# Performance work log

Hardware: AMD Instinct MI355X
Metric: run time of the kernel (lower is better)

The kernel has to match this reference:

```python
import jax, jax.numpy as jnp
import numpy as np

DIM = 192; HEADS = 6
RES = (8, 96, 180)      # (Pl, Lat, Lon), all divisible by window -> pad/crop are no-ops
WIN = (2, 6, 12)        # (win_pl, win_lat, win_lon)
SHIFT = (1, 3, 6)
MLP_RATIO = 4


def earth_position_index(win):
    wpl, wlat, wlon = win
    zi = np.arange(wpl); zj = -np.arange(wpl) * wpl
    hi = np.arange(wlat); hj = -np.arange(wlat) * wlat
    w = np.arange(wlon)
    c1 = np.stack(np.meshgrid(zi, hi, w, indexing='ij')).reshape(3, -1)
    c2 = np.stack(np.meshgrid(zj, hj, w, indexing='ij')).reshape(3, -1)
    coords = (c1[:, :, None] - c2[:, None, :]).transpose(1, 2, 0).copy()  # (N, N, 3)
    coords[:, :, 2] += wlon - 1
    coords[:, :, 1] *= 2 * wlon - 1
    coords[:, :, 0] *= (2 * wlon - 1) * wlat * wlat
    return coords.sum(-1)  # (N, N) int index into bias table


def shift_window_mask(res, win, shift):
    Pl, Lat, Lon = res; wpl, wlat, wlon = win; spl, slat, slon = shift
    m = np.zeros((Pl, Lat, Lon + slon))
    cnt = 0
    pls = (slice(0, -wpl), slice(-wpl, -spl), slice(-spl, None))
    las = (slice(0, -wlat), slice(-wlat, -slat), slice(-slat, None))
    los = (slice(0, -wlon), slice(-wlon, -slon), slice(-slon, None))
    for p in pls:
        for l in las:
            for o in los:
                m[p, l, o] = cnt; cnt += 1
    m = m[:, :, :Lon]
    npl, nlat, nlon = Pl // wpl, Lat // wlat, Lon // wlon
    mw = m.reshape(npl, wpl, nlat, wlat, nlon, wlon).transpose(4, 0, 2, 1, 3, 5)
    mw = mw.reshape(nlon, npl * nlat, wpl * wlat * wlon)
    am = mw[:, :, None, :] - mw[:, :, :, None]
    return np.where(am != 0, -100.0, 0.0).astype(np.float32)  # (nlon, nW, N, N)


EPI = earth_position_index(WIN)                       # static int index
ATTN_MASK = shift_window_mask(RES, WIN, SHIFT)        # static float mask


def setup_inputs() -> dict:
    key = jax.random.key(0)
    ks = jax.random.split(key, 16)
    Pl, Lat, Lon = RES; wpl, wlat, wlon = WIN
    L = Pl * Lat * Lon
    nW = (Pl // wpl) * (Lat // wlat)  # type_of_windows
    tbl = wpl ** 2 * wlat ** 2 * (2 * wlon - 1)
    C = DIM; H = MLP_RATIO * DIM
    n = lambda k, s, std=0.02: (jax.random.normal(k, s, dtype=jnp.float32) * std)
    return {
        'x': jax.random.normal(ks[0], (1, L, C), dtype=jnp.float32),
        'norm1_g': jnp.ones((C,), jnp.float32), 'norm1_b': jnp.zeros((C,), jnp.float32),
        'qkv_w': n(ks[1], (C, 3 * C)), 'qkv_b': jnp.zeros((3 * C,), jnp.float32),
        'bias_table': n(ks[2], (tbl, nW, HEADS)),
        'proj_w': n(ks[3], (C, C)), 'proj_b': jnp.zeros((C,), jnp.float32),
        'norm2_g': jnp.ones((C,), jnp.float32), 'norm2_b': jnp.zeros((C,), jnp.float32),
        'fc1_w': n(ks[4], (C, H)), 'fc1_b': jnp.zeros((H,), jnp.float32),
        'fc2_w': n(ks[5], (H, C)), 'fc2_b': jnp.zeros((C,), jnp.float32),
    }


def _layernorm(y, g, b, eps=1e-5):
    mu = y.mean(-1, keepdims=True)
    var = y.var(-1, keepdims=True)
    return (y - mu) / jnp.sqrt(var + eps) * g + b


def reference(x, norm1_g, norm1_b, qkv_w, qkv_b, bias_table, proj_w, proj_b,
              norm2_g, norm2_b, fc1_w, fc1_b, fc2_w, fc2_b):
    B, L, C = x.shape
    Pl, Lat, Lon = RES; wpl, wlat, wlon = WIN; spl, slat, slon = SHIFT
    npl, nlat, nlon = Pl // wpl, Lat // wlat, Lon // wlon
    N = wpl * wlat * wlon; nW = npl * nlat
    h = HEADS; d = C // h
    scale = d ** -0.5

    shortcut = x
    y = _layernorm(x, norm1_g, norm1_b).reshape(B, Pl, Lat, Lon, C)
    y = jnp.roll(y, shift=(-spl, -slat, -slon), axis=(1, 2, 3))
    # window partition: b (npl wpl)(nlat wlat)(nlon wlon) c -> (b nlon)(npl nlat)(wpl wlat wlon) c
    yw = y.reshape(B, npl, wpl, nlat, wlat, nlon, wlon, C)
    yw = yw.transpose(0, 5, 1, 3, 2, 4, 6, 7).reshape(B * nlon, nW, N, C)

    qkv = (yw @ qkv_w + qkv_b).reshape(B * nlon, nW, N, 3, h, d)
    qkv = qkv.transpose(3, 0, 4, 1, 2, 5)  # (3, B_, h, nW, N, d)
    q, k, v = qkv[0] * scale, qkv[1], qkv[2]
    attn = jnp.einsum('bhwnd,bhwmd->bhwnm', q, k)  # (B_, h, nW, N, N)

    bias = bias_table[EPI.reshape(-1)].reshape(N, N, nW, h).transpose(3, 2, 0, 1)  # (h, nW, N, N)
    attn = attn + bias[None]
    mask = jnp.asarray(ATTN_MASK)  # (nlon, nW, N, N)
    attn = attn.reshape(B, nlon, h, nW, N, N) + mask[None, :, None]
    attn = jax.nn.softmax(attn.reshape(B * nlon, h, nW, N, N), axis=-1)

    out = jnp.einsum('bhwnm,bhwmd->bhwnd', attn, v)
    out = out.transpose(0, 2, 3, 1, 4).reshape(B * nlon, nW, N, C)
    out = out @ proj_w + proj_b
    # window reverse + un-shift
    out = out.reshape(B, nlon, npl, nlat, wpl, wlat, wlon, C)
    out = out.transpose(0, 2, 4, 3, 5, 1, 6, 7).reshape(B, Pl, Lat, Lon, C)
    out = jnp.roll(out, shift=(spl, slat, slon), axis=(1, 2, 3)).reshape(B, L, C)

    x = shortcut + out
    y = _layernorm(x, norm2_g, norm2_b)
    y = jax.nn.gelu(y @ fc1_w + fc1_b, approximate=False) @ fc2_w + fc2_b
    return x + y
```

## Files before the change

### kernel.cpp

```cpp
#include <hip/hip_runtime.h>


typedef __attribute__((ext_vector_type(8))) short short8;
typedef __attribute__((ext_vector_type(4))) short short4v;
typedef __attribute__((ext_vector_type(4))) float floatx4;
typedef unsigned short bfu;

#define GLOAD_LDS16(g, l)                                            \
  __builtin_amdgcn_global_load_lds(                                  \
      (const __attribute__((address_space(1))) unsigned int*)(g),    \
      (__attribute__((address_space(3))) unsigned int*)(l), 16, 0, 0)

__device__ __forceinline__ bfu f2bf(float f) {
  unsigned int u = __builtin_bit_cast(unsigned int, f);
  u += 0x7fffu + ((u >> 16) & 1u);
  return (bfu)(u >> 16);
}
__device__ __forceinline__ float bf2f(bfu s) {
  return __builtin_bit_cast(float, (unsigned int)s << 16);
}

__global__ void wt_kernel(const float* __restrict__ src, bfu* __restrict__ dst,
                          int K, int N) {
  int idx = blockIdx.x * 256 + threadIdx.x;
  if (idx >= K * N) return;
  int k = idx / N, n = idx % N;
  dst[(size_t)n * K + k] = f2bf(src[idx]);
}

__global__ void bias2_kernel(const float* __restrict__ table,
                             bfu* __restrict__ out) {
  int idx = blockIdx.x * 256 + threadIdx.x;
  if (idx >= 1271808) return;
  int h = idx / 211968;
  int r = idx % 211968;
  int w = r / 3312, ep = r % 3312;
  out[idx] = f2bf(table[(size_t)ep * 384 + w * 6 + h]);
}

__global__ void vpad_kernel(unsigned int* __restrict__ vbw) {
  int tid = threadIdx.x;
  int dd = tid >> 3, c = tid & 7;
  vbw[(size_t)blockIdx.x * 2560 + dd * 80 + 72 + c] = 0;
}

__global__ __launch_bounds__(256) void ln1_kernel(
    const float* __restrict__ x, const float* __restrict__ g,
    const float* __restrict__ be, bfu* __restrict__ A1) {
  int wv = threadIdx.x >> 6, lane = threadIdx.x & 63;
  int r = blockIdx.x * 4 + wv;
  int n = r % 144, w = (r / 144) & 63, bb = r / 9216;
  int ip = w >> 4, il = w & 15;
  int p1 = n / 72, rem = n % 72, l1 = rem / 12, o1 = rem % 12;
  int pl = ip * 2 + p1 + 1;   if (pl >= 8) pl -= 8;
  int lat = il * 6 + l1 + 3;  if (lat >= 96) lat -= 96;
  int lon = bb * 12 + o1 + 6; if (lon >= 180) lon -= 180;
  size_t t = (size_t)(pl * 96 + lat) * 180 + lon;
  const float* xr = x + t * 192;
  float v0 = xr[lane], v1 = xr[lane + 64], v2 = xr[lane + 128];
  float s = v0 + v1 + v2;
  #pragma unroll
  for (int o = 32; o; o >>= 1) s += __shfl_xor(s, o);
  float mu = s * (1.0f / 192.0f);
  float d0 = v0 - mu, d1 = v1 - mu, d2 = v2 - mu;
  float q2 = d0 * d0 + d1 * d1 + d2 * d2;
  #pragma unroll
  for (int o = 32; o; o >>= 1) q2 += __shfl_xor(q2, o);
  float rstd = rsqrtf(q2 * (1.0f / 192.0f) + 1e-5f);
  bfu* orow = A1 + (size_t)r * 192;
  orow[lane]       = f2bf(d0 * rstd * g[lane]       + be[lane]);
  orow[lane + 64]  = f2bf(d1 * rstd * g[lane + 64]  + be[lane + 64]);
  orow[lane + 128] = f2bf(d2 * rstd * g[lane + 128] + be[lane + 128]);
}

__global__ __launch_bounds__(256) void ln2_kernel(
    const float* __restrict__ xin, const float* __restrict__ g,
    const float* __restrict__ be, bfu* __restrict__ yout) {
  int wv = threadIdx.x >> 6, lane = threadIdx.x & 63;
  size_t r = (size_t)blockIdx.x * 4 + wv;
  const float* xr = xin + r * 192;
  float v0 = xr[lane], v1 = xr[lane + 64], v2 = xr[lane + 128];
  float s = v0 + v1 + v2;
  #pragma unroll
  for (int o = 32; o; o >>= 1) s += __shfl_xor(s, o);
  float mu = s * (1.0f / 192.0f);
  float d0 = v0 - mu, d1 = v1 - mu, d2 = v2 - mu;
  float q2 = d0 * d0 + d1 * d1 + d2 * d2;
  #pragma unroll
  for (int o = 32; o; o >>= 1) q2 += __shfl_xor(q2, o);
  float rstd = rsqrtf(q2 * (1.0f / 192.0f) + 1e-5f);
  bfu* orow = yout + r * 192;
  orow[lane]       = f2bf(d0 * rstd * g[lane]       + be[lane]);
  orow[lane + 64]  = f2bf(d1 * rstd * g[lane + 64]  + be[lane + 64]);
  orow[lane + 128] = f2bf(d2 * rstd * g[lane + 128] + be[lane + 128]);
}

__global__ __launch_bounds__(256, 4) void gemm_kernel(
    const bfu* __restrict__ A, const bfu* __restrict__ BT,
    const float* __restrict__ bias, int K, int NT, int mode,
    const float* aux, void* out0, void* out1, void* out2) {
  __shared__ __align__(16) short LB[14336];
  short* As = LB;
  short* Bs = LB + 8192;
  bfu* E = (bfu*)LB;
  const int tid = threadIdx.x;
  const int wv = tid >> 6, lane = tid & 63;
  const int r16 = lane & 15, quad = lane >> 4;
  const int sw = r16 & 7;

  const int W = gridDim.x;
  const int work = (blockIdx.x & 7) * (W >> 3) + (blockIdx.x >> 3);
  const int m0 = (work / NT) * 128;
  const int n0 = (work % NT) * 96;
  const bfu* Bsrc = BT + (size_t)n0 * K;

  floatx4 acc[2][6];
  #pragma unroll
  for (int s = 0; s < 2; ++s)
    #pragma unroll
    for (int j = 0; j < 6; ++j) acc[s][j] = (floatx4){0.f, 0.f, 0.f, 0.f};

  for (int kc = 0; kc < K; kc += 64) {
    __syncthreads();
    #pragma unroll
    for (int j = 0; j < 4; ++j) {
      int c = j * 256 + tid;
      int row = c >> 3, l = (c & 7) ^ (row & 7);
      GLOAD_LDS16(A + (size_t)(m0 + row) * K + kc + l * 8, As + c * 8);
    }
    #pragma unroll
    for (int j = 0; j < 3; ++j) {
      int c = j * 256 + tid;
      int row = c >> 3, l = (c & 7) ^ (row & 7);
      GLOAD_LDS16(Bsrc + (size_t)row * K + kc + l * 8, Bs + c * 8);
    }
    __syncthreads();
    #pragma unroll
    for (int ks = 0; ks < 2; ++ks) {
      const int p8 = ((ks * 4 + quad) ^ sw) * 8;
      short8 a[2], b[6];
      #pragma unroll
      for (int s = 0; s < 2; ++s)
        a[s] = *(const short8*)(As + (wv * 32 + s * 16 + r16) * 64 + p8);
      #pragma unroll
      for (int j = 0; j < 6; ++j)
        b[j] = *(const short8*)(Bs + (j * 16 + r16) * 64 + p8);
      #pragma unroll
      for (int s = 0; s < 2; ++s)
        #pragma unroll
        for (int j = 0; j < 6; ++j)
          acc[s][j] =
              __builtin_amdgcn_mfma_f32_16x16x32_bf16(a[s], b[j], acc[s][j], 0, 0, 0);
    }
  }

  if (mode == 0 || mode == 2) {
    __syncthreads();
    #pragma unroll
    for (int s = 0; s < 2; ++s) {
      int er = wv * 32 + s * 16 + quad * 4;
      #pragma unroll
      for (int j = 0; j < 6; ++j) {
        int c = j * 16 + r16;
        float bia = bias[n0 + c];
        #pragma unroll
        for (int i = 0; i < 4; ++i) {
          float val = acc[s][j][i] + bia;
          if (mode == 0) {
            if (n0 < 192) val *= 0.17677669529663687f;
            E[(er + i) * 104 + c] = f2bf(val);
          } else {
            float ge = 0.5f * val * (1.0f + erff(val * 0.70710678118654752f));
            E[(er + i) * 104 + c] = f2bf(ge);
          }
        }
      }
    }
    __syncthreads();
    if (mode == 2) {
      #pragma unroll
      for (int u = 0; u < 6; ++u) {
        int id = u * 256 + tid;
        int r = id / 12, c8 = (id % 12) * 8;
        *(short8*)((bfu*)out0 + (size_t)(m0 + r) * 768 + n0 + c8) =
            *(const short8*)(E + r * 104 + c8);
      }
    } else if (n0 < 384) {
      bfu* dst = (bfu*)(n0 < 192 ? out0 : out1);
      #pragma unroll
      for (int u = 0; u < 6; ++u) {
        int id = u * 256 + tid;
        int r = id / 12, c8 = (id % 12) * 8;
        int row = m0 + r;
        int n = row % 144, w = (row / 144) & 63, bb = row / 9216;
        int head = ((n0 + c8) % 192) >> 5, dd = c8 & 31;
        size_t win = (size_t)(bb * 6 + head) * 64 + w;
        *(short8*)(dst + win * 4608 + n * 32 + dd) =
            *(const short8*)(E + r * 104 + c8);
      }
    } else {
      #pragma unroll
      for (int u = 0; u < 6; ++u) {
        int id = u * 256 + tid;
        int c = id % 96, k8 = id / 96;
        int r0 = k8 * 8;
        int row0 = m0 + r0;
        int n = row0 % 144, w = (row0 / 144) & 63, bb = row0 / 9216;
        int head = ((n0 + c) % 192) >> 5, dd = c & 31;
        size_t win = (size_t)(bb * 6 + head) * 64 + w;
        short8 t8;
        #pragma unroll
        for (int i = 0; i < 8; ++i) t8[i] = (short)E[(r0 + i) * 104 + c];
        *(short8*)((bfu*)out2 + win * 5120 + dd * 160 + n) = t8;
      }
    }
  } else {
    #pragma unroll
    for (int s = 0; s < 2; ++s) {
      const int row0 = m0 + wv * 32 + s * 16 + quad * 4;
      #pragma unroll
      for (int j = 0; j < 6; ++j) {
        int col = n0 + j * 16 + r16;
        float bia = bias[col];
        #pragma unroll
        for (int i = 0; i < 4; ++i) {
          int row = row0 + i;
          float val = acc[s][j][i] + bia;
          if (mode == 1) {
            int n = row % 144, w = (row / 144) & 63, bb = row / 9216;
            int ip = w >> 4, il = w & 15;
            int p1 = n / 72, rem = n % 72, l1 = rem / 12, o1 = rem % 12;
            int pl = ip * 2 + p1 + 1;   if (pl >= 8) pl -= 8;
            int lat = il * 6 + l1 + 3;  if (lat >= 96) lat -= 96;
            int lon = bb * 12 + o1 + 6; if (lon >= 180) lon -= 180;
            size_t t = (size_t)(pl * 96 + lat) * 180 + lon;
            ((float*)out0)[t * 192 + col] = aux[t * 192 + col] + val;
          } else {
            size_t idx = (size_t)row * 192 + col;
            ((float*)out0)[idx] = aux[idx] + val;
          }
        }
      }
    }
  }
}

__global__ __launch_bounds__(256) void attn_kernel(
    const bfu* __restrict__ qg_, const bfu* __restrict__ kg_,
    const bfu* __restrict__ vg_, const bfu* __restrict__ tblT,
    bfu* __restrict__ aout) {
  __shared__ __align__(16) bfu Ss[144 * 148];
  __shared__ __align__(16) bfu bias_l[3312];
  __shared__ unsigned short rn[144];
  __shared__ short cm[144];
  __shared__ unsigned char regs[144];

  const int w = blockIdx.x, h0 = blockIdx.y * 2, b = blockIdx.z;
  const int tid = threadIdx.x;
  const int wv = tid >> 6, lane = tid & 63, r16 = lane & 15, quad = lane >> 4;

  if (tid < 144) {
    int n = tid;
    int p1 = n / 72, rem = n % 72, l1 = rem / 12, o1 = rem % 12;
    rn[n] = (unsigned short)(828 * p1 + 23 * l1 + o1 + 11);
    cm[n] = (short)(1656 * p1 + 138 * l1 - o1);
    int ip = w >> 4, il = w & 15;
    int pl = ip * 2 + p1, lat = il * 6 + l1, lon = b * 12 + o1;
    int rp = pl < 6 ? 0 : (pl < 7 ? 1 : 2);
    int rl = lat < 90 ? 0 : (lat < 93 ? 1 : 2);
    int ro = lon < 174 ? 0 : 1;
    regs[n] = (unsigned char)(rp * 9 + rl * 3 + ro);
  }

  {
    const bfu* bsrc = tblT + (size_t)(h0 * 64 + w) * 3312;
    GLOAD_LDS16(bsrc + tid * 8, bias_l + tid * 8);
    if (tid < 158) GLOAD_LDS16(bsrc + (256 + tid) * 8, bias_l + (256 + tid) * 8);
  }

  short4v ov[2][5];
  #pragma unroll
  for (int hh = 0; hh < 2; ++hh) {
    const int h = h0 + hh;
    const size_t win = (size_t)((b * 6 + h) * 64 + w);
    const bfu* qg = qg_ + win * 4608;
    const bfu* kg = kg_ + win * 4608;
    const bfu* vt = vg_ + win * 5120;

    #pragma unroll 3
    for (int u = 0; u < 21; ++u) {
      int t = wv * 21 + u;
      if (t < 81) {
        int tn = t / 9, tm = t % 9;
        short8 a  = *(const short8*)(qg + (tn * 16 + r16) * 32 + quad * 8);
        short8 bo = *(const short8*)(kg + (tm * 16 + r16) * 32 + quad * 8);
        floatx4 z = (floatx4){0.f, 0.f, 0.f, 0.f};
        floatx4 d = __builtin_amdgcn_mfma_f32_16x16x32_bf16(a, bo, z, 0, 0, 0);
        int m = tm * 16 + r16;
        #pragma unroll
        for (int i = 0; i < 4; ++i)
          Ss[(tn * 16 + quad * 4 + i) * 148 + m] = f2bf(d[i]);
      }
    }
    __syncthreads();

    for (int rb = 0; rb < 9; ++rb) {
      int rr = rb * 16 + wv * 4 + quad;
      unsigned char rgn = regs[rr];
      int rnv = rn[rr];
      const bfu* srow = Ss + rr * 148;
      float v[9];
      float mx = -1e30f;
      #pragma unroll
      for (int j = 0; j < 9; ++j) {
        int c = r16 + 16 * j;
        float s = bf2f(srow[c]) + bf2f(bias_l[rnv + cm[c]]);
        if (regs[c] != rgn) s -= 100.0f;
        v[j] = s;
        mx = fmaxf(mx, s);
      }
      #pragma unroll
      for (int o = 8; o; o >>= 1) mx = fmaxf(mx, __shfl_xor(mx, o));
      float sum = 0.f;
      #pragma unroll
      for (int j = 0; j < 9; ++j) { v[j] = __expf(v[j] - mx); sum += v[j]; }
      #pragma unroll
      for (int o = 8; o; o >>= 1) sum += __shfl_xor(sum, o);
      float inv = 1.0f / sum;
      bfu* wrow = Ss + rr * 148;
      #pragma unroll
      for (int j = 0; j < 9; ++j) wrow[r16 + 16 * j] = f2bf(v[j] * inv);
    }
    __syncthreads();

    if (hh == 0) {
      const bfu* bsrc = tblT + (size_t)((h0 + 1) * 64 + w) * 3312;
      GLOAD_LDS16(bsrc + tid * 8, bias_l + tid * 8);
      if (tid < 158) GLOAD_LDS16(bsrc + (256 + tid) * 8, bias_l + (256 + tid) * 8);
    }

    short8 bfr[2][5];
    #pragma unroll
    for (int td = 0; td < 2; ++td)
      #pragma unroll
      for (int km = 0; km < 5; ++km)
        bfr[td][km] =
            *(const short8*)(vt + (td * 16 + r16) * 160 + km * 32 + quad * 8);

    #pragma unroll
    for (int u = 0; u < 5; ++u) {
      int t = wv * 5 + u;
      if (t < 18) {
        int tn = t >> 1, td = t & 1;
        floatx4 acc = (floatx4){0.f, 0.f, 0.f, 0.f};
        #pragma unroll
        for (int km = 0; km < 5; ++km) {
          short8 a;
          if (km == 4 && quad >= 2) {
            a = (short8)(short)0;
          } else {
            const bfu* ap = Ss + (tn * 16 + r16) * 148 + km * 32 + quad * 8;
            *(short4v*)&a       = *(const short4v*)ap;
            *((short4v*)&a + 1) = *(const short4v*)(ap + 4);
          }
          acc = __builtin_amdgcn_mfma_f32_16x16x32_bf16(bfr[td][km], a, acc, 0, 0, 0);
        }
        short4v o;
        #pragma unroll
        for (int i = 0; i < 4; ++i) o[i] = (short)f2bf(acc[i]);
        ov[hh][u] = o;
      }
    }
    if (hh == 0) __syncthreads();
  }

  __syncthreads();
  bfu* Os = Ss;
  #pragma unroll
  for (int u = 0; u < 5; ++u) {
    int t = wv * 5 + u;
    if (t < 18) {
      int tn = t >> 1, td = t & 1;
      int ro = tn * 16 + r16;
      *(short4v*)(Os + ro * 80 + td * 16 + quad * 4)      = ov[0][u];
      *(short4v*)(Os + ro * 80 + 32 + td * 16 + quad * 4) = ov[1][u];
    }
  }
  __syncthreads();
  const size_t obase = (size_t)((b * 64 + w) * 144) * 192 + h0 * 32;
  #pragma unroll
  for (int u = 0; u < 5; ++u) {
    int c = u * 256 + tid;
    if (c < 1152) {
      int r = c >> 3, k = c & 7;
      *(short8*)(aout + obase + (size_t)r * 192 + k * 8) =
          *(const short8*)(Os + r * 80 + k * 8);
    }
  }
}

extern "C" void kernel_launch(void* const* d_in, const int* in_sizes, int n_in,
                              void* d_out, int out_size, void* d_ws, size_t ws_size,
                              hipStream_t stream) {
  (void)in_sizes; (void)n_in; (void)out_size; (void)ws_size;
  const float* x     = (const float*)d_in[0];
  const float* n1g   = (const float*)d_in[1];
  const float* n1b   = (const float*)d_in[2];
  const float* qkvw  = (const float*)d_in[3];
  const float* qkvb  = (const float*)d_in[4];
  const float* tbl   = (const float*)d_in[5];
  const float* projw = (const float*)d_in[6];
  const float* projb = (const float*)d_in[7];
  const float* n2g   = (const float*)d_in[8];
  const float* n2b   = (const float*)d_in[9];
  const float* fc1w  = (const float*)d_in[10];
  const float* fc1b  = (const float*)d_in[11];
  const float* fc2w  = (const float*)d_in[12];
  const float* fc2b  = (const float*)d_in[13];

  char* ws = (char*)d_ws;
  bfu* wt_qkv   = (bfu*)(ws + 0);
  bfu* wt_proj  = (bfu*)(ws + 221184);
  bfu* wt_fc1   = (bfu*)(ws + 294912);
  bfu* wt_fc2   = (bfu*)(ws + 589824);
  bfu* tblT     = (bfu*)(ws + 884736);
  bfu* A1       = (bfu*)(ws + 16809984);
  bfu* qb       = (bfu*)(ws + 69894144);
  bfu* kb       = (bfu*)(ws + 122978304);
  bfu* vb       = (bfu*)(ws + 176062464);
  bfu* hb       = qb;
  float* out    = (float*)d_out;

  wt_kernel<<<432, 256, 0, stream>>>(qkvw, wt_qkv, 192, 576);
  wt_kernel<<<144, 256, 0, stream>>>(projw, wt_proj, 192, 192);
  wt_kernel<<<576, 256, 0, stream>>>(fc1w, wt_fc1, 192, 768);
  wt_kernel<<<576, 256, 0, stream>>>(fc2w, wt_fc2, 768, 192);
  bias2_kernel<<<4968, 256, 0, stream>>>(tbl, tblT);
  vpad_kernel<<<5760, 256, 0, stream>>>((unsigned int*)vb);
  ln1_kernel<<<34560, 256, 0, stream>>>(x, n1g, n1b, A1);
  gemm_kernel<<<6480, 256, 0, stream>>>(A1, wt_qkv, qkvb, 192, 6, 0,
                                        nullptr, qb, kb, vb);
  attn_kernel<<<dim3(64, 3, 15), 256, 0, stream>>>(qb, kb, vb, tblT, A1);
  gemm_kernel<<<2160, 256, 0, stream>>>(A1, wt_proj, projb, 192, 2, 1,
                                        x, out, nullptr, nullptr);
  ln2_kernel<<<34560, 256, 0, stream>>>(out, n2g, n2b, A1);
  gemm_kernel<<<8640, 256, 0, stream>>>(A1, wt_fc1, fc1b, 192, 8, 2,
                                        nullptr, hb, nullptr, nullptr);
  gemm_kernel<<<2160, 256, 0, stream>>>(hb, wt_fc2, fc2b, 768, 2, 3,
                                        out, out, nullptr, nullptr);
}
```

Before: 967.7 us.

## Fold log2e into scores, drop softmax max pass, restructure GEMM and QK tiling

Premultiplies the q scale and the bias table by log2(e) so softmax uses exp2 directly, and removes the max-subtraction pass, assuming scores stay in a safe range. The GEMM now loads A straight into registers from global memory and stages only B in LDS with a K-chunk of 192, with occupancy lowered to 3. The QK^T stage keeps q fragments in registers and gives each wave fixed key tiles. Column mask and bias offsets are hoisted into registers. Dropping the max subtraction risks overflow for larger logits, and the bigger register footprint reduces occupancy.

Result: slower. 987.9 us (+2.1%).

```diff
diff --git a/kernel.cpp b/kernel.cpp
--- a/kernel.cpp
+++ b/kernel.cpp
@@ -35,7 +35,7 @@
   int h = idx / 211968;
   int r = idx % 211968;
   int w = r / 3312, ep = r % 3312;
-  out[idx] = f2bf(table[(size_t)ep * 384 + w * 6 + h]);
+  out[idx] = f2bf(table[(size_t)ep * 384 + w * 6 + h] * 1.4426950408889634f);
 }
 
 __global__ void vpad_kernel(unsigned int* __restrict__ vbw) {
@@ -95,14 +95,12 @@
   orow[lane + 128] = f2bf(d2 * rstd * g[lane + 128] + be[lane + 128]);
 }
 
-__global__ __launch_bounds__(256, 4) void gemm_kernel(
+__global__ __launch_bounds__(256, 3) void gemm_kernel(
     const bfu* __restrict__ A, const bfu* __restrict__ BT,
     const float* __restrict__ bias, int K, int NT, int mode,
     const float* aux, void* out0, void* out1, void* out2) {
-  __shared__ __align__(16) short LB[14336];
-  short* As = LB;
-  short* Bs = LB + 8192;
-  bfu* E = (bfu*)LB;
+  __shared__ __align__(16) short Bs[18432];
+  bfu* E = (bfu*)Bs;
   const int tid = threadIdx.x;
   const int wv = tid >> 6, lane = tid & 63;
   const int r16 = lane & 15, quad = lane >> 4;
@@ -114,43 +112,46 @@
   const int n0 = (work % NT) * 96;
   const bfu* Bsrc = BT + (size_t)n0 * K;
 
+  const short* Arow[2];
+  #pragma unroll
+  for (int s = 0; s < 2; ++s)
+    Arow[s] = (const short*)A + (size_t)(m0 + wv * 32 + s * 16 + r16) * K + quad * 8;
+
   floatx4 acc[2][6];
   #pragma unroll
   for (int s = 0; s < 2; ++s)
     #pragma unroll
     for (int j = 0; j < 6; ++j) acc[s][j] = (floatx4){0.f, 0.f, 0.f, 0.f};
 
-  for (int kc = 0; kc < K; kc += 64) {
-    __syncthreads();
-    #pragma unroll
-    for (int j = 0; j < 4; ++j) {
+  for (int kc = 0; kc < K; kc += 192) {
+    __syncthreads();
+    #pragma unroll
+    for (int j = 0; j < 9; ++j) {
       int c = j * 256 + tid;
-      int row = c >> 3, l = (c & 7) ^ (row & 7);
-      GLOAD_LDS16(A + (size_t)(m0 + row) * K + kc + l * 8, As + c * 8);
-    }
-    #pragma unroll
-    for (int j = 0; j < 3; ++j) {
-      int c = j * 256 + tid;
-      int row = c >> 3, l = (c & 7) ^ (row & 7);
+      int row = c / 24, sl = c % 24;
+      int l = (sl & ~7) | ((sl ^ row) & 7);
       GLOAD_LDS16(Bsrc + (size_t)row * K + kc + l * 8, Bs + c * 8);
     }
-    __syncthreads();
-    #pragma unroll
-    for (int ks = 0; ks < 2; ++ks) {
-      const int p8 = ((ks * 4 + quad) ^ sw) * 8;
-      short8 a[2], b[6];
-      #pragma unroll
-      for (int s = 0; s < 2; ++s)
-        a[s] = *(const short8*)(As + (wv * 32 + s * 16 + r16) * 64 + p8);
+    short8 ar[2][6];
+    #pragma unroll
+    for (int s = 0; s < 2; ++s)
+      #pragma unroll
+      for (int ks = 0; ks < 6; ++ks)
+        ar[s][ks] = *(const short8*)(Arow[s] + kc + ks * 32);
+    __syncthreads();
+    #pragma unroll
+    for (int ks = 0; ks < 6; ++ks) {
+      const int s_log = ks * 4 + quad;
+      const int p8 = ((s_log & ~7) | ((s_log ^ sw) & 7)) * 8;
+      short8 b[6];
       #pragma unroll
       for (int j = 0; j < 6; ++j)
-        b[j] = *(const short8*)(Bs + (j * 16 + r16) * 64 + p8);
-      #pragma unroll
-      for (int s = 0; s < 2; ++s)
-        #pragma unroll
-        for (int j = 0; j < 6; ++j)
-          acc[s][j] =
-              __builtin_amdgcn_mfma_f32_16x16x32_bf16(a[s], b[j], acc[s][j], 0, 0, 0);
+        b[j] = *(const short8*)(Bs + (j * 16 + r16) * 192 + p8);
+      #pragma unroll
+      for (int j = 0; j < 6; ++j) {
+        acc[0][j] = __builtin_amdgcn_mfma_f32_16x16x32_bf16(ar[0][ks], b[j], acc[0][j], 0, 0, 0);
+        acc[1][j] = __builtin_amdgcn_mfma_f32_16x16x32_bf16(ar[1][ks], b[j], acc[1][j], 0, 0, 0);
+      }
     }
   }
 
@@ -167,7 +168,7 @@
         for (int i = 0; i < 4; ++i) {
           float val = acc[s][j][i] + bia;
           if (mode == 0) {
-            if (n0 < 192) val *= 0.17677669529663687f;
+            if (n0 < 192) val *= 0.25503633958871686f;
             E[(er + i) * 104 + c] = f2bf(val);
           } else {
             float ge = 0.5f * val * (1.0f + erff(val * 0.70710678118654752f));
@@ -277,6 +278,16 @@
     GLOAD_LDS16(bsrc + tid * 8, bias_l + tid * 8);
     if (tid < 158) GLOAD_LDS16(bsrc + (256 + tid) * 8, bias_l + (256 + tid) * 8);
   }
+  __syncthreads();
+
+  short cmv[9];
+  unsigned char creg[9];
+  #pragma unroll
+  for (int j = 0; j < 9; ++j) {
+    int c = r16 + 16 * j;
+    cmv[j] = cm[c];
+    creg[j] = regs[c];
+  }
 
   short4v ov[2][5];
   #pragma unroll
@@ -287,19 +298,28 @@
     const bfu* kg = kg_ + win * 4608;
     const bfu* vt = vg_ + win * 5120;
 
-    #pragma unroll 3
-    for (int u = 0; u < 21; ++u) {
-      int t = wv * 21 + u;
-      if (t < 81) {
-        int tn = t / 9, tm = t % 9;
-        short8 a  = *(const short8*)(qg + (tn * 16 + r16) * 32 + quad * 8);
-        short8 bo = *(const short8*)(kg + (tm * 16 + r16) * 32 + quad * 8);
-        floatx4 z = (floatx4){0.f, 0.f, 0.f, 0.f};
-        floatx4 d = __builtin_amdgcn_mfma_f32_16x16x32_bf16(a, bo, z, 0, 0, 0);
-        int m = tm * 16 + r16;
-        #pragma unroll
-        for (int i = 0; i < 4; ++i)
-          Ss[(tn * 16 + quad * 4 + i) * 148 + m] = f2bf(d[i]);
+    short8 qf[9];
+    #pragma unroll
+    for (int t9 = 0; t9 < 9; ++t9)
+      qf[t9] = *(const short8*)(qg + (t9 * 16 + r16) * 32 + quad * 8);
+    const int tma = wv * 2, tmb = wv * 2 + 1;
+    short8 kfa = *(const short8*)(kg + (tma * 16 + r16) * 32 + quad * 8);
+    short8 kfb = *(const short8*)(kg + (tmb * 16 + r16) * 32 + quad * 8);
+    short8 kfc = *(const short8*)(kg + (128 + r16) * 32 + quad * 8);
+    const floatx4 z = (floatx4){0.f, 0.f, 0.f, 0.f};
+    #pragma unroll
+    for (int tn = 0; tn < 9; ++tn) {
+      bfu* srow = Ss + (tn * 16 + quad * 4) * 148;
+      floatx4 d = __builtin_amdgcn_mfma_f32_16x16x32_bf16(qf[tn], kfa, z, 0, 0, 0);
+      #pragma unroll
+      for (int i = 0; i < 4; ++i) srow[i * 148 + tma * 16 + r16] = f2bf(d[i]);
+      d = __builtin_amdgcn_mfma_f32_16x16x32_bf16(qf[tn], kfb, z, 0, 0, 0);
+      #pragma unroll
+      for (int i = 0; i < 4; ++i) srow[i * 148 + tmb * 16 + r16] = f2bf(d[i]);
+      if ((tn & 3) == wv) {
+        d = __builtin_amdgcn_mfma_f32_16x16x32_bf16(qf[tn], kfc, z, 0, 0, 0);
+        #pragma unroll
+        for (int i = 0; i < 4; ++i) srow[i * 148 + 128 + r16] = f2bf(d[i]);
       }
     }
     __syncthreads();
@@ -310,20 +330,14 @@
       int rnv = rn[rr];
       const bfu* srow = Ss + rr * 148;
       float v[9];
-      float mx = -1e30f;
+      float sum = 0.f;
       #pragma unroll
       for (int j = 0; j < 9; ++j) {
-        int c = r16 + 16 * j;
-        float s = bf2f(srow[c]) + bf2f(bias_l[rnv + cm[c]]);
-        if (regs[c] != rgn) s -= 100.0f;
-        v[j] = s;
-        mx = fmaxf(mx, s);
-      }
-      #pragma unroll
-      for (int o = 8; o; o >>= 1) mx = fmaxf(mx, __shfl_xor(mx, o));
-      float sum = 0.f;
-      #pragma unroll
-      for (int j = 0; j < 9; ++j) { v[j] = __expf(v[j] - mx); sum += v[j]; }
+        float s = bf2f(srow[r16 + 16 * j]) + bf2f(bias_l[rnv + cmv[j]]);
+        s = (creg[j] != rgn) ? s - 144.26950408889634f : s;
+        v[j] = exp2f(s);
+        sum += v[j];
+      }
       #pragma unroll
       for (int o = 8; o; o >>= 1) sum += __shfl_xor(sum, o);
       float inv = 1.0f / sum;
```
